# Optimization experiments

Hardware: AMD Instinct MI355X
Metric: run time of the kernel (lower is better)

## Reference

```python
import jax, jax.numpy as jnp
import numpy as np

B, S, D, H = 2, 2048, 1024, 16
DH = D // H  # head dim = 64


def setup_inputs() -> dict:
    key0 = jax.random.key(0)
    ks = jax.random.split(key0, 12)
    wscale = 0.02
    inp = {
        "query": jax.random.normal(ks[0], (B, S, D), jnp.float32),
        "key": jax.random.normal(ks[1], (B, S, D), jnp.float32),
        "value": jax.random.normal(ks[2], (B, S, D), jnp.float32),
        "mask": jnp.zeros((B, 1, 1, S), jnp.float32),  # 1.0 = masked position
        "Wq": jax.random.normal(ks[3], (D, D), jnp.float32) * wscale,
        "bq": jnp.zeros((D,), jnp.float32),
        "Wk": jax.random.normal(ks[4], (D, D), jnp.float32) * wscale,
        "bk": jnp.zeros((D,), jnp.float32),
        "Wv": jax.random.normal(ks[5], (D, D), jnp.float32) * wscale,
        "bv": jnp.zeros((D,), jnp.float32),
        "Wo": jax.random.normal(ks[6], (D, D), jnp.float32) * wscale,
        "bo": jnp.zeros((D,), jnp.float32),
        "batch_size": B,
    }
    return inp


def _split_heads(x, batch_size):
    # [B, S, D] -> [B, H, S, DH]
    return x.reshape(batch_size, -1, H, DH).transpose(0, 2, 1, 3)


def reference(query, key, value, mask, Wq, bq, Wk, bk, Wv, bv, Wo, bo, batch_size):
    q = _split_heads(query @ Wq + bq, batch_size)  # [B,H,S,DH]
    k = _split_heads(key @ Wk + bk, batch_size)
    v = _split_heads(value @ Wv + bv, batch_size)

    scale = 1.0 / jnp.sqrt(jnp.asarray(DH, q.dtype))
    scores = jnp.einsum("bhqd,bhkd->bhqk", q, k) * scale  # [B,H,S,S]
    scores = scores + mask * jnp.asarray(-1e9, scores.dtype)
    attn = jax.nn.softmax(scores, axis=-1)
    ctx = jnp.einsum("bhqk,bhkd->bhqd", attn, v)  # [B,H,S,DH]

    ctx = ctx.transpose(0, 2, 1, 3).reshape(batch_size, -1, D)  # [B,S,D]
    return ctx @ Wo + bo
```

## Files before the change

### kernel.cpp

```cpp
#include <hip/hip_runtime.h>
#include <hip/hip_bf16.h>

#define BB 2
#define SS 2048
#define DD 1024
#define HH 16
#define DHH 64
#define MM (BB * SS)

typedef unsigned short u16;
using v8s   = __attribute__((ext_vector_type(8))) short;
using f32x4 = __attribute__((ext_vector_type(4))) float;

#define LOG2E 1.44269504088896340736f

__device__ __forceinline__ u16 f2bf(float f) {
  unsigned int u = __float_as_uint(f);
  u += 0x7fffu + ((u >> 16) & 1u);
  return (u16)(u >> 16);
}

__device__ __forceinline__ unsigned int pk2(float a, float b) {
  __hip_bfloat162 h = __float22bfloat162_rn(float2{a, b});
  return *(unsigned int*)&h;
}

__device__ __forceinline__ void async_cp16(const u16* g, u16* l) {
  __builtin_amdgcn_global_load_lds(
      (const __attribute__((address_space(1))) unsigned int*)g,
      (__attribute__((address_space(3))) unsigned int*)l, 16, 0, 0);
}

__global__ __launch_bounds__(256) void conv_all(const float* __restrict__ x0,
                                                const float* __restrict__ x1,
                                                const float* __restrict__ x2,
                                                u16* __restrict__ y0,
                                                u16* __restrict__ y1,
                                                u16* __restrict__ y2) {
  const int z = blockIdx.y;
  const float* x = z == 0 ? x0 : (z == 1 ? x1 : x2);
  u16* y = z == 0 ? y0 : (z == 1 ? y1 : y2);
  int i = (blockIdx.x * 256 + threadIdx.x) * 4;
  float4 v = *(const float4*)(x + i);
  uint2 u;
  u.x = pk2(v.x, v.y);
  u.y = pk2(v.z, v.w);
  *(uint2*)(y + i) = u;
}

__global__ __launch_bounds__(256) void trans_all(
    const float* __restrict__ W0, const float* __restrict__ W1,
    const float* __restrict__ W2, const float* __restrict__ W3,
    u16* __restrict__ T0, u16* __restrict__ T1,
    u16* __restrict__ T2, u16* __restrict__ T3) {
  const int z = blockIdx.z;
  const float* W = z == 0 ? W0 : (z == 1 ? W1 : (z == 2 ? W2 : W3));
  u16* Wt = z == 0 ? T0 : (z == 1 ? T1 : (z == 2 ? T2 : T3));
  __shared__ u16 T[64][72];
  const int tid = threadIdx.x;
  const int k0 = blockIdx.y * 64, n0 = blockIdx.x * 64;
#pragma unroll
  for (int i = 0; i < 4; i++) {
    int idx = tid + i * 256;
    int r = idx >> 4, c = (idx & 15) * 4;
    float4 x = *(const float4*)(W + (long)(k0 + r) * DD + n0 + c);
    T[c + 0][r] = f2bf(x.x);
    T[c + 1][r] = f2bf(x.y);
    T[c + 2][r] = f2bf(x.z);
    T[c + 3][r] = f2bf(x.w);
  }
  __syncthreads();
#pragma unroll
  for (int i = 0; i < 2; i++) {
    int idx = tid + i * 256;
    int n = idx >> 3, kc = (idx & 7) * 8;
    *(v8s*)(Wt + (long)(n0 + n) * DD + k0 + kc) = *(const v8s*)&T[n][kc];
  }
}

__global__ __launch_bounds__(256, 2) void proj_fused(
    const u16* __restrict__ qb, const u16* __restrict__ kb, const u16* __restrict__ vb,
    const u16* __restrict__ Wqt, const u16* __restrict__ Wkt, const u16* __restrict__ Wvt,
    const float* __restrict__ bq, const float* __restrict__ bk, const float* __restrict__ bv,
    u16* __restrict__ qo, u16* __restrict__ ko, u16* __restrict__ vo) {
  __shared__ union ShU {
    struct { u16 As[128 * 32]; u16 Bs[128 * 32]; } st;
    u16 T[128 * 136];
  } sh;
  const int z = blockIdx.z;
  const u16* A  = z == 0 ? qb : (z == 1 ? kb : vb);
  const u16* Bt = z == 0 ? Wqt : (z == 1 ? Wkt : Wvt);
  const float* bias = z == 0 ? bq : (z == 1 ? bk : bv);
  u16* out = z == 0 ? qo : (z == 1 ? ko : vo);
  const float scale = z == 0 ? 0.125f * LOG2E : 1.0f;

  const int tid = threadIdx.x;
  const int w = tid >> 6, lane = tid & 63;
  const int quad = lane >> 4, lq = lane & 15;
  const int wm = w >> 1, wn = w & 1;
  const int row0 = blockIdx.y * 128, col0 = blockIdx.x * 128;

  f32x4 acc[4][4];
#pragma unroll
  for (int i = 0; i < 4; i++)
#pragma unroll
    for (int j = 0; j < 4; j++)
#pragma unroll
      for (int r = 0; r < 4; r++) acc[i][j][r] = 0.f;

  const int cr = tid >> 2, cc = (tid & 3) * 8;

  for (int k0 = 0; k0 < DD; k0 += 32) {
    __syncthreads();
    async_cp16(A  + (long)(row0 + cr) * DD + k0 + cc,      sh.st.As + (w * 64) * 8);
    async_cp16(A  + (long)(row0 + 64 + cr) * DD + k0 + cc, sh.st.As + (256 + w * 64) * 8);
    async_cp16(Bt + (long)(col0 + cr) * DD + k0 + cc,      sh.st.Bs + (w * 64) * 8);
    async_cp16(Bt + (long)(col0 + 64 + cr) * DD + k0 + cc, sh.st.Bs + (256 + w * 64) * 8);
    __syncthreads();

    v8s a[4], b[4];
#pragma unroll
    for (int i = 0; i < 4; i++)
      a[i] = *(const v8s*)&sh.st.As[(wm * 64 + i * 16 + lq) * 32 + quad * 8];
#pragma unroll
    for (int j = 0; j < 4; j++)
      b[j] = *(const v8s*)&sh.st.Bs[(wn * 64 + j * 16 + lq) * 32 + quad * 8];
#pragma unroll
    for (int i = 0; i < 4; i++)
#pragma unroll
      for (int j = 0; j < 4; j++)
        acc[i][j] = __builtin_amdgcn_mfma_f32_16x16x32_bf16(a[i], b[j], acc[i][j], 0, 0, 0);
  }

  __syncthreads();

  if (z != 2) {
#pragma unroll
    for (int j = 0; j < 4; j++) {
      int nl = wn * 64 + j * 16 + lq;
      float bi = bias[col0 + nl];
#pragma unroll
      for (int i = 0; i < 4; i++)
#pragma unroll
        for (int r = 0; r < 4; r++) {
          int ml = wm * 64 + i * 16 + quad * 4 + r;
          sh.T[ml * 136 + nl] = f2bf((acc[i][j][r] + bi) * scale);
        }
    }
    __syncthreads();
    const int bb = row0 >> 11;
#pragma unroll
    for (int t = 0; t < 8; t++) {
      int c = tid + t * 256;
      int m = c >> 4, jc = c & 15;
      int s = (row0 + m) & (SS - 1);
      int gn = col0 + jc * 8;
      int hh = gn >> 6, d = gn & (DHH - 1);
      long off = ((long)(bb * HH + hh) * SS + s) * DHH + d;
      *(v8s*)(out + off) = *(const v8s*)&sh.T[m * 136 + jc * 8];
    }
  } else {
#pragma unroll
    for (int j = 0; j < 4; j++) {
      int nl = wn * 64 + j * 16 + lq;
      float bi = bias[col0 + nl];
#pragma unroll
      for (int i = 0; i < 4; i++) {
        int ml = wm * 64 + i * 16 + quad * 4;
        uint2 pk;
        pk.x = pk2(acc[i][j][0] + bi, acc[i][j][1] + bi);
        pk.y = pk2(acc[i][j][2] + bi, acc[i][j][3] + bi);
        *(uint2*)&sh.T[nl * 136 + ml] = pk;
      }
    }
    __syncthreads();
    const int bb = row0 >> 11;
#pragma unroll
    for (int t = 0; t < 8; t++) {
      int c = tid + t * 256;
      int n = c >> 4, jc = c & 15;
      int gn = col0 + n;
      int hh = gn >> 6, d = gn & (DHH - 1);
      int s = (row0 + jc * 8) & (SS - 1);
      long off = ((long)(bb * HH + hh) * DHH + d) * SS + s;
      *(v8s*)(out + off) = *(const v8s*)&sh.T[n * 136 + jc * 8];
    }
  }
}

__global__ __launch_bounds__(256, 2) void out_gemm(const u16* __restrict__ A,
                                                   const u16* __restrict__ Bt,
                                                   const float* __restrict__ bias,
                                                   float* __restrict__ outp) {
  __shared__ u16 As[64 * 32];
  __shared__ u16 Bs[128 * 32];
  const int tid = threadIdx.x;
  const int w = tid >> 6, lane = tid & 63;
  const int quad = lane >> 4, lq = lane & 15;
  const int wm = w >> 1, wn = w & 1;
  const int row0 = blockIdx.y * 64, col0 = blockIdx.x * 128;

  f32x4 acc[2][4];
#pragma unroll
  for (int i = 0; i < 2; i++)
#pragma unroll
    for (int j = 0; j < 4; j++)
#pragma unroll
      for (int r = 0; r < 4; r++) acc[i][j][r] = 0.f;

  const int cr = tid >> 2, cc = (tid & 3) * 8;

  for (int k0 = 0; k0 < DD; k0 += 32) {
    __syncthreads();
    async_cp16(A  + (long)(row0 + cr) * DD + k0 + cc,      As + (w * 64) * 8);
    async_cp16(Bt + (long)(col0 + cr) * DD + k0 + cc,      Bs + (w * 64) * 8);
    async_cp16(Bt + (long)(col0 + 64 + cr) * DD + k0 + cc, Bs + (256 + w * 64) * 8);
    __syncthreads();

    v8s a[2], b[4];
#pragma unroll
    for (int i = 0; i < 2; i++)
      a[i] = *(const v8s*)&As[(wm * 32 + i * 16 + lq) * 32 + quad * 8];
#pragma unroll
    for (int j = 0; j < 4; j++)
      b[j] = *(const v8s*)&Bs[(wn * 64 + j * 16 + lq) * 32 + quad * 8];
#pragma unroll
    for (int i = 0; i < 2; i++)
#pragma unroll
      for (int j = 0; j < 4; j++)
        acc[i][j] = __builtin_amdgcn_mfma_f32_16x16x32_bf16(a[i], b[j], acc[i][j], 0, 0, 0);
  }

#pragma unroll
  for (int i = 0; i < 2; i++)
#pragma unroll
    for (int j = 0; j < 4; j++) {
      int n = col0 + wn * 64 + j * 16 + lq;
      float bi = bias[n];
#pragma unroll
      for (int r = 0; r < 4; r++) {
        int m = row0 + wm * 32 + i * 16 + quad * 4 + r;
        outp[(long)m * DD + n] = acc[i][j][r] + bi;
      }
    }
}

__global__ __launch_bounds__(256, 2) void attn_flash(
    const u16* __restrict__ qg, const u16* __restrict__ kg,
    const u16* __restrict__ vg, const float* __restrict__ mask,
    u16* __restrict__ ctx) {
  __shared__ u16 Ks[128 * 72];
  __shared__ u16 Vs[64 * 136];
  __shared__ u16 Pts[128 * 136];
  __shared__ float mneg[128];

  const int tid = threadIdx.x;
  const int w = tid >> 6, lane = tid & 63;
  const int quad = lane >> 4, lq = lane & 15;
  const int q0 = blockIdx.x * 128;
  const int h = blockIdx.y, b = blockIdx.z;
  const long hoff = (long)(b * HH + h) * SS * DHH;

  v8s aq[2][2];
#pragma unroll
  for (int qs_ = 0; qs_ < 2; qs_++)
#pragma unroll
    for (int ks_ = 0; ks_ < 2; ks_++)
      aq[qs_][ks_] = *(const v8s*)(qg + hoff +
          (long)(q0 + w * 32 + qs_ * 16 + lq) * DHH + ks_ * 32 + quad * 8);

  f32x4 o[2][4];
  float l_i[2] = {0.f, 0.f};
#pragma unroll
  for (int a = 0; a < 2; a++)
#pragma unroll
    for (int n_ = 0; n_ < 4; n_++)
#pragma unroll
      for (int r = 0; r < 4; r++) o[a][n_][r] = 0.f;

  for (int kv0 = 0; kv0 < SS; kv0 += 128) {
    __syncthreads();
#pragma unroll
    for (int t = 0; t < 4; t++) {
      int c = tid + t * 256;
      *(v8s*)&Ks[(c >> 3) * 72 + (c & 7) * 8] =
          *(const v8s*)(kg + hoff + (long)(kv0 + (c >> 3)) * DHH + (c & 7) * 8);
      *(v8s*)&Vs[(c >> 4) * 136 + (c & 15) * 8] =
          *(const v8s*)(vg + hoff + (long)(c >> 4) * SS + kv0 + (c & 15) * 8);
    }
    if (tid < 32) {
      float4 mm = *(const float4*)(mask + (long)b * SS + kv0 + tid * 4);
      mneg[tid * 4 + 0] = (mm.x * -1e9f - 4.0f) * LOG2E;
      mneg[tid * 4 + 1] = (mm.y * -1e9f - 4.0f) * LOG2E;
      mneg[tid * 4 + 2] = (mm.z * -1e9f - 4.0f) * LOG2E;
      mneg[tid * 4 + 3] = (mm.w * -1e9f - 4.0f) * LOG2E;
    }
    __syncthreads();

    f32x4 sc[2][8];
#pragma unroll
    for (int qs_ = 0; qs_ < 2; qs_++)
#pragma unroll
      for (int kv_ = 0; kv_ < 8; kv_++)
#pragma unroll
        for (int r = 0; r < 4; r++) sc[qs_][kv_][r] = 0.f;
#pragma unroll
    for (int ks_ = 0; ks_ < 2; ks_++)
#pragma unroll
      for (int kv_ = 0; kv_ < 8; kv_++) {
        v8s ak = *(const v8s*)&Ks[(kv_ * 16 + lq) * 72 + ks_ * 32 + quad * 8];
        sc[0][kv_] = __builtin_amdgcn_mfma_f32_16x16x32_bf16(ak, aq[0][ks_], sc[0][kv_], 0, 0, 0);
        sc[1][kv_] = __builtin_amdgcn_mfma_f32_16x16x32_bf16(ak, aq[1][ks_], sc[1][kv_], 0, 0, 0);
      }

#pragma unroll
    for (int qs_ = 0; qs_ < 2; qs_++) {
      float lsum = 0.f;
      const int prow = (w * 32 + qs_ * 16 + lq) * 136;
#pragma unroll
      for (int kv_ = 0; kv_ < 8; kv_++) {
        f32x4 mv = *(const f32x4*)&mneg[kv_ * 16 + quad * 4];
        float p0 = exp2f(sc[qs_][kv_][0] + mv[0]);
        float p1 = exp2f(sc[qs_][kv_][1] + mv[1]);
        float p2 = exp2f(sc[qs_][kv_][2] + mv[2]);
        float p3 = exp2f(sc[qs_][kv_][3] + mv[3]);
        lsum += (p0 + p1) + (p2 + p3);
        uint2 pk;
        pk.x = pk2(p0, p1);
        pk.y = pk2(p2, p3);
        *(uint2*)&Pts[prow + kv_ * 16 + quad * 4] = pk;
      }
      l_i[qs_] += lsum;
    }

#pragma unroll
    for (int ks2 = 0; ks2 < 4; ks2++) {
      v8s bv[4];
#pragma unroll
      for (int n_ = 0; n_ < 4; n_++)
        bv[n_] = *(const v8s*)&Vs[(n_ * 16 + lq) * 136 + ks2 * 32 + quad * 8];
#pragma unroll
      for (int qs_ = 0; qs_ < 2; qs_++) {
        v8s ap = *(const v8s*)&Pts[(w * 32 + qs_ * 16 + lq) * 136 + ks2 * 32 + quad * 8];
#pragma unroll
        for (int n_ = 0; n_ < 4; n_++)
          o[qs_][n_] = __builtin_amdgcn_mfma_f32_16x16x32_bf16(ap, bv[n_], o[qs_][n_], 0, 0, 0);
      }
    }
  }

#pragma unroll
  for (int qs_ = 0; qs_ < 2; qs_++) {
    float l = l_i[qs_];
    l += __shfl_xor(l, 16);
    l += __shfl_xor(l, 32);
    float inv = 1.0f / l;
    float ir[4];
    ir[0] = __shfl(inv, quad * 4 + 0);
    ir[1] = __shfl(inv, quad * 4 + 1);
    ir[2] = __shfl(inv, quad * 4 + 2);
    ir[3] = __shfl(inv, quad * 4 + 3);
#pragma unroll
    for (int r = 0; r < 4; r++) {
      int s = q0 + w * 32 + qs_ * 16 + quad * 4 + r;
      long base = (long)(b * SS + s) * DD + h * DHH;
#pragma unroll
      for (int n_ = 0; n_ < 4; n_++)
        ctx[base + n_ * 16 + lq] = f2bf(o[qs_][n_][r] * ir[r]);
    }
  }
}

extern "C" void kernel_launch(void* const* d_in, const int* in_sizes, int n_in,
                              void* d_out, int out_size, void* d_ws, size_t ws_size,
                              hipStream_t stream) {
  const float* query = (const float*)d_in[0];
  const float* key   = (const float*)d_in[1];
  const float* value = (const float*)d_in[2];
  const float* mask  = (const float*)d_in[3];
  const float* Wq = (const float*)d_in[4];
  const float* bq = (const float*)d_in[5];
  const float* Wk = (const float*)d_in[6];
  const float* bk = (const float*)d_in[7];
  const float* Wv = (const float*)d_in[8];
  const float* bv = (const float*)d_in[9];
  const float* Wo = (const float*)d_in[10];
  const float* bo = (const float*)d_in[11];

  u16* ws = (u16*)d_ws;
  const long A4 = (long)MM * DD;
  const long W1 = (long)DD * DD;
  u16* qb  = ws;
  u16* kb  = ws + A4;
  u16* vb  = ws + 2 * A4;
  u16* Wqt = ws + 3 * A4;
  u16* Wkt = Wqt + W1;
  u16* Wvt = Wkt + W1;
  u16* Wot = Wvt + W1;
  u16* q_ws   = ws + 3 * A4 + 4 * W1;
  u16* k_ws   = q_ws + A4;
  u16* v_ws   = k_ws + A4;
  u16* ctx_ws = v_ws + A4;

  conv_all<<<dim3(A4 / 1024, 3), 256, 0, stream>>>(query, key, value, qb, kb, vb);
  trans_all<<<dim3(16, 16, 4), 256, 0, stream>>>(Wq, Wk, Wv, Wo, Wqt, Wkt, Wvt, Wot);

  proj_fused<<<dim3(DD / 128, MM / 128, 3), 256, 0, stream>>>(
      qb, kb, vb, Wqt, Wkt, Wvt, bq, bk, bv, q_ws, k_ws, v_ws);

  attn_flash<<<dim3(SS / 128, HH, BB), 256, 0, stream>>>(q_ws, k_ws, v_ws, mask, ctx_ws);

  out_gemm<<<dim3(DD / 128, MM / 64), 256, 0, stream>>>(ctx_ws, Wot, bo, (float*)d_out);
}
```

Before: 251.8 us.

## Deepen GEMM K-tiles to 64, swizzle attention LDS, use raw exp2 builtin

The projection and output GEMMs now stage a K-slice of 64 per iteration instead of 32, which halves the number of barrier pairs per tile but doubles LDS staging. The attention kernel replaces padded LDS rows with an XOR swizzle for K, V and P tiles, shrinking shared memory while aiming to avoid bank conflicts. The softmax exponent switches to the raw hardware exp2 builtin, with a fallback to __expf that rescales Q and the mask. The larger GEMM LDS footprint could reduce occupancy, and the unswizzled GEMM tiles with a 64-element row stride may see more bank conflicts.

```diff
diff --git a/kernel.cpp b/kernel.cpp
--- a/kernel.cpp
+++ b/kernel.cpp
@@ -14,6 +14,16 @@
 
 #define LOG2E 1.44269504088896340736f
 
+#if __has_builtin(__builtin_amdgcn_exp2f)
+#define EXP_RAW(x) __builtin_amdgcn_exp2f(x)
+#define QSCALE (0.125f * LOG2E)
+#define MSCALE LOG2E
+#else
+#define EXP_RAW(x) __expf(x)
+#define QSCALE 0.125f
+#define MSCALE 1.0f
+#endif
+
 __device__ __forceinline__ u16 f2bf(float f) {
   unsigned int u = __float_as_uint(f);
   u += 0x7fffu + ((u >> 16) & 1u);
@@ -29,6 +39,10 @@
   __builtin_amdgcn_global_load_lds(
       (const __attribute__((address_space(1))) unsigned int*)g,
       (__attribute__((address_space(3))) unsigned int*)l, 16, 0, 0);
+}
+
+__device__ __forceinline__ int swz(int r, int c8) {
+  return (c8 & ~7) | ((c8 ^ r) & 7);
 }
 
 __global__ __launch_bounds__(256) void conv_all(const float* __restrict__ x0,
@@ -84,7 +98,7 @@
     const float* __restrict__ bq, const float* __restrict__ bk, const float* __restrict__ bv,
     u16* __restrict__ qo, u16* __restrict__ ko, u16* __restrict__ vo) {
   __shared__ union ShU {
-    struct { u16 As[128 * 32]; u16 Bs[128 * 32]; } st;
+    struct { u16 As[128 * 64]; u16 Bs[128 * 64]; } st;
     u16 T[128 * 136];
   } sh;
   const int z = blockIdx.z;
@@ -92,7 +106,7 @@
   const u16* Bt = z == 0 ? Wqt : (z == 1 ? Wkt : Wvt);
   const float* bias = z == 0 ? bq : (z == 1 ? bk : bv);
   u16* out = z == 0 ? qo : (z == 1 ? ko : vo);
-  const float scale = z == 0 ? 0.125f * LOG2E : 1.0f;
+  const float scale = z == 0 ? QSCALE : 1.0f;
 
   const int tid = threadIdx.x;
   const int w = tid >> 6, lane = tid & 63;
@@ -108,28 +122,34 @@
 #pragma unroll
       for (int r = 0; r < 4; r++) acc[i][j][r] = 0.f;
 
-  const int cr = tid >> 2, cc = (tid & 3) * 8;
-
-  for (int k0 = 0; k0 < DD; k0 += 32) {
-    __syncthreads();
-    async_cp16(A  + (long)(row0 + cr) * DD + k0 + cc,      sh.st.As + (w * 64) * 8);
-    async_cp16(A  + (long)(row0 + 64 + cr) * DD + k0 + cc, sh.st.As + (256 + w * 64) * 8);
-    async_cp16(Bt + (long)(col0 + cr) * DD + k0 + cc,      sh.st.Bs + (w * 64) * 8);
-    async_cp16(Bt + (long)(col0 + 64 + cr) * DD + k0 + cc, sh.st.Bs + (256 + w * 64) * 8);
-    __syncthreads();
-
-    v8s a[4], b[4];
-#pragma unroll
-    for (int i = 0; i < 4; i++)
-      a[i] = *(const v8s*)&sh.st.As[(wm * 64 + i * 16 + lq) * 32 + quad * 8];
-#pragma unroll
-    for (int j = 0; j < 4; j++)
-      b[j] = *(const v8s*)&sh.st.Bs[(wn * 64 + j * 16 + lq) * 32 + quad * 8];
-#pragma unroll
-    for (int i = 0; i < 4; i++)
+  const int cr = tid >> 3, cc = (tid & 7) * 8;
+
+  for (int k0 = 0; k0 < DD; k0 += 64) {
+    __syncthreads();
+#pragma unroll
+    for (int it = 0; it < 4; it++) {
+      async_cp16(A  + (long)(row0 + cr + it * 32) * DD + k0 + cc,
+                 sh.st.As + (it * 256 + w * 64) * 8);
+      async_cp16(Bt + (long)(col0 + cr + it * 32) * DD + k0 + cc,
+                 sh.st.Bs + (it * 256 + w * 64) * 8);
+    }
+    __syncthreads();
+
+#pragma unroll
+    for (int kk = 0; kk < 2; kk++) {
+      v8s a[4], b[4];
+#pragma unroll
+      for (int i = 0; i < 4; i++)
+        a[i] = *(const v8s*)&sh.st.As[(wm * 64 + i * 16 + lq) * 64 + kk * 32 + quad * 8];
 #pragma unroll
       for (int j = 0; j < 4; j++)
-        acc[i][j] = __builtin_amdgcn_mfma_f32_16x16x32_bf16(a[i], b[j], acc[i][j], 0, 0, 0);
+        b[j] = *(const v8s*)&sh.st.Bs[(wn * 64 + j * 16 + lq) * 64 + kk * 32 + quad * 8];
+#pragma unroll
+      for (int i = 0; i < 4; i++)
+#pragma unroll
+        for (int j = 0; j < 4; j++)
+          acc[i][j] = __builtin_amdgcn_mfma_f32_16x16x32_bf16(a[i], b[j], acc[i][j], 0, 0, 0);
+    }
   }
 
   __syncthreads();
@@ -192,8 +212,8 @@
                                                    const u16* __restrict__ Bt,
                                                    const float* __restrict__ bias,
                                                    float* __restrict__ outp) {
-  __shared__ u16 As[64 * 32];
-  __shared__ u16 Bs[128 * 32];
+  __shared__ u16 As[64 * 64];
+  __shared__ u16 Bs[128 * 64];
   const int tid = threadIdx.x;
   const int w = tid >> 6, lane = tid & 63;
   const int quad = lane >> 4, lq = lane & 15;
@@ -208,27 +228,35 @@
 #pragma unroll
       for (int r = 0; r < 4; r++) acc[i][j][r] = 0.f;
 
-  const int cr = tid >> 2, cc = (tid & 3) * 8;
-
-  for (int k0 = 0; k0 < DD; k0 += 32) {
-    __syncthreads();
-    async_cp16(A  + (long)(row0 + cr) * DD + k0 + cc,      As + (w * 64) * 8);
-    async_cp16(Bt + (long)(col0 + cr) * DD + k0 + cc,      Bs + (w * 64) * 8);
-    async_cp16(Bt + (long)(col0 + 64 + cr) * DD + k0 + cc, Bs + (256 + w * 64) * 8);
-    __syncthreads();
-
-    v8s a[2], b[4];
-#pragma unroll
-    for (int i = 0; i < 2; i++)
-      a[i] = *(const v8s*)&As[(wm * 32 + i * 16 + lq) * 32 + quad * 8];
-#pragma unroll
-    for (int j = 0; j < 4; j++)
-      b[j] = *(const v8s*)&Bs[(wn * 64 + j * 16 + lq) * 32 + quad * 8];
-#pragma unroll
-    for (int i = 0; i < 2; i++)
+  const int cr = tid >> 3, cc = (tid & 7) * 8;
+
+  for (int k0 = 0; k0 < DD; k0 += 64) {
+    __syncthreads();
+#pragma unroll
+    for (int it = 0; it < 2; it++)
+      async_cp16(A + (long)(row0 + cr + it * 32) * DD + k0 + cc,
+                 As + (it * 256 + w * 64) * 8);
+#pragma unroll
+    for (int it = 0; it < 4; it++)
+      async_cp16(Bt + (long)(col0 + cr + it * 32) * DD + k0 + cc,
+                 Bs + (it * 256 + w * 64) * 8);
+    __syncthreads();
+
+#pragma unroll
+    for (int kk = 0; kk < 2; kk++) {
+      v8s a[2], b[4];
+#pragma unroll
+      for (int i = 0; i < 2; i++)
+        a[i] = *(const v8s*)&As[(wm * 32 + i * 16 + lq) * 64 + kk * 32 + quad * 8];
 #pragma unroll
       for (int j = 0; j < 4; j++)
-        acc[i][j] = __builtin_amdgcn_mfma_f32_16x16x32_bf16(a[i], b[j], acc[i][j], 0, 0, 0);
+        b[j] = *(const v8s*)&Bs[(wn * 64 + j * 16 + lq) * 64 + kk * 32 + quad * 8];
+#pragma unroll
+      for (int i = 0; i < 2; i++)
+#pragma unroll
+        for (int j = 0; j < 4; j++)
+          acc[i][j] = __builtin_amdgcn_mfma_f32_16x16x32_bf16(a[i], b[j], acc[i][j], 0, 0, 0);
+    }
   }
 
 #pragma unroll
@@ -249,9 +277,9 @@
     const u16* __restrict__ qg, const u16* __restrict__ kg,
     const u16* __restrict__ vg, const float* __restrict__ mask,
     u16* __restrict__ ctx) {
-  __shared__ u16 Ks[128 * 72];
-  __shared__ u16 Vs[64 * 136];
-  __shared__ u16 Pts[128 * 136];
+  __shared__ u16 Ks[128 * 64];
+  __shared__ u16 Vs[64 * 128];
+  __shared__ u16 Pts[128 * 128];
   __shared__ float mneg[128];
 
   const int tid = threadIdx.x;
@@ -283,17 +311,19 @@
 #pragma unroll
     for (int t = 0; t < 4; t++) {
       int c = tid + t * 256;
-      *(v8s*)&Ks[(c >> 3) * 72 + (c & 7) * 8] =
-          *(const v8s*)(kg + hoff + (long)(kv0 + (c >> 3)) * DHH + (c & 7) * 8);
-      *(v8s*)&Vs[(c >> 4) * 136 + (c & 15) * 8] =
-          *(const v8s*)(vg + hoff + (long)(c >> 4) * SS + kv0 + (c & 15) * 8);
+      int rk = c >> 3, ck = c & 7;
+      *(v8s*)&Ks[rk * 64 + swz(rk, ck) * 8] =
+          *(const v8s*)(kg + hoff + (long)(kv0 + rk) * DHH + ck * 8);
+      int rv = c >> 4, cv = c & 15;
+      *(v8s*)&Vs[rv * 128 + swz(rv, cv) * 8] =
+          *(const v8s*)(vg + hoff + (long)rv * SS + kv0 + cv * 8);
     }
     if (tid < 32) {
       float4 mm = *(const float4*)(mask + (long)b * SS + kv0 + tid * 4);
-      mneg[tid * 4 + 0] = (mm.x * -1e9f - 4.0f) * LOG2E;
-      mneg[tid * 4 + 1] = (mm.y * -1e9f - 4.0f) * LOG2E;
-      mneg[tid * 4 + 2] = (mm.z * -1e9f - 4.0f) * LOG2E;
-      mneg[tid * 4 + 3] = (mm.w * -1e9f - 4.0f) * LOG2E;
+      mneg[tid * 4 + 0] = (mm.x * -1e9f - 4.0f) * MSCALE;
+      mneg[tid * 4 + 1] = (mm.y * -1e9f - 4.0f) * MSCALE;
+      mneg[tid * 4 + 2] = (mm.z * -1e9f - 4.0f) * MSCALE;
+      mneg[tid * 4 + 3] = (mm.w * -1e9f - 4.0f) * MSCALE;
     }
     __syncthreads();
 
@@ -308,7 +338,8 @@
     for (int ks_ = 0; ks_ < 2; ks_++)
 #pragma unroll
       for (int kv_ = 0; kv_ < 8; kv_++) {
-        v8s ak = *(const v8s*)&Ks[(kv_ * 16 + lq) * 72 + ks_ * 32 + quad * 8];
+        int rk = kv_ * 16 + lq;
+        v8s ak = *(const v8s*)&Ks[rk * 64 + swz(rk, ks_ * 4 + quad) * 8];
         sc[0][kv_] = __builtin_amdgcn_mfma_f32_16x16x32_bf16(ak, aq[0][ks_], sc[0][kv_], 0, 0, 0);
         sc[1][kv_] = __builtin_amdgcn_mfma_f32_16x16x32_bf16(ak, aq[1][ks_], sc[1][kv_], 0, 0, 0);
       }
@@ -316,19 +347,20 @@
 #pragma unroll
     for (int qs_ = 0; qs_ < 2; qs_++) {
       float lsum = 0.f;
-      const int prow = (w * 32 + qs_ * 16 + lq) * 136;
+      const int qrow = w * 32 + qs_ * 16 + lq;
 #pragma unroll
       for (int kv_ = 0; kv_ < 8; kv_++) {
         f32x4 mv = *(const f32x4*)&mneg[kv_ * 16 + quad * 4];
-        float p0 = exp2f(sc[qs_][kv_][0] + mv[0]);
-        float p1 = exp2f(sc[qs_][kv_][1] + mv[1]);
-        float p2 = exp2f(sc[qs_][kv_][2] + mv[2]);
-        float p3 = exp2f(sc[qs_][kv_][3] + mv[3]);
+        float p0 = EXP_RAW(sc[qs_][kv_][0] + mv[0]);
+        float p1 = EXP_RAW(sc[qs_][kv_][1] + mv[1]);
+        float p2 = EXP_RAW(sc[qs_][kv_][2] + mv[2]);
+        float p3 = EXP_RAW(sc[qs_][kv_][3] + mv[3]);
         lsum += (p0 + p1) + (p2 + p3);
         uint2 pk;
         pk.x = pk2(p0, p1);
         pk.y = pk2(p2, p3);
-        *(uint2*)&Pts[prow + kv_ * 16 + quad * 4] = pk;
+        int c8 = kv_ * 2 + (quad >> 1);
+        *(uint2*)&Pts[qrow * 128 + swz(qrow, c8) * 8 + (quad & 1) * 4] = pk;
       }
       l_i[qs_] += lsum;
     }
@@ -337,11 +369,14 @@
     for (int ks2 = 0; ks2 < 4; ks2++) {
       v8s bv[4];
 #pragma unroll
-      for (int n_ = 0; n_ < 4; n_++)
-        bv[n_] = *(const v8s*)&Vs[(n_ * 16 + lq) * 136 + ks2 * 32 + quad * 8];
+      for (int n_ = 0; n_ < 4; n_++) {
+        int rv = n_ * 16 + lq;
+        bv[n_] = *(const v8s*)&Vs[rv * 128 + swz(rv, ks2 * 4 + quad) * 8];
+      }
 #pragma unroll
       for (int qs_ = 0; qs_ < 2; qs_++) {
-        v8s ap = *(const v8s*)&Pts[(w * 32 + qs_ * 16 + lq) * 136 + ks2 * 32 + quad * 8];
+        int qrow = w * 32 + qs_ * 16 + lq;
+        v8s ap = *(const v8s*)&Pts[qrow * 128 + swz(qrow, ks2 * 4 + quad) * 8];
 #pragma unroll
         for (int n_ = 0; n_ < 4; n_++)
           o[qs_][n_] = __builtin_amdgcn_mfma_f32_16x16x32_bf16(ap, bv[n_], o[qs_][n_], 0, 0, 0);
```

New measurement: 236.9 us. 5.9% less time.
